# Optimization experiments

Hardware: AMD Instinct MI355X
Metric: run time of the kernel (lower is better)

The kernel has to match this reference:

```python
import jax, jax.numpy as jnp
import numpy as np

EPS = 1e-5
L = 256
CHANNELS = 256


def setup_inputs() -> dict:
    key = jax.random.key(0)
    ks = jax.random.split(key, 7)
    B, C, D, H, W = 2, 256, 48, 48, 48
    x = jax.random.normal(ks[0], (B, C, D, H, W), dtype=jnp.float32)
    # Conv1d(kernel=1) weights: [out_channels, in_channels], plus bias.
    s = 1.0 / np.sqrt(C)
    Wq = jax.random.uniform(ks[1], (CHANNELS, C), jnp.float32, -s, s)
    bq = jax.random.uniform(ks[2], (CHANNELS,), jnp.float32, -s, s)
    Wk = jax.random.uniform(ks[3], (CHANNELS, C), jnp.float32, -s, s)
    bk = jax.random.uniform(ks[4], (CHANNELS,), jnp.float32, -s, s)
    Wv = jax.random.uniform(ks[5], (CHANNELS, C), jnp.float32, -s, s)
    bv = jax.random.uniform(ks[6], (CHANNELS,), jnp.float32, -s, s)
    outer = jnp.eye(L, dtype=jnp.float32)  # learned, init = identity
    return {"x": x, "Wq": Wq, "bq": bq, "Wk": Wk, "bk": bk, "Wv": Wv, "bv": bv, "outer": outer}


def reference(x, Wq, bq, Wk, bk, Wv, bv, outer):
    B, C, D, H, W = x.shape
    N = D * H * W
    # InstanceNorm3d (affine=False): normalize per (B, C) over spatial dims, biased var.
    xf = x.reshape(B, C, N)
    mean = jnp.mean(xf, axis=-1, keepdims=True)
    var = jnp.mean(jnp.square(xf - mean), axis=-1, keepdims=True)
    xn = (xf - mean) * jax.lax.rsqrt(var + EPS)  # [B, C, N]
    # 1x1 Conv1d projections == GEMM over channel dim.
    q = jnp.einsum('oc,bcn->bon', Wq, xn) + bq[None, :, None]
    k = jnp.einsum('oc,bcn->bon', Wk, xn) + bk[None, :, None]
    v = jnp.einsum('oc,bcn->bon', Wv, xn) + bv[None, :, None]
    # Channel attention: scores [B, C, C]; scale applied AFTER softmax.
    scores = jnp.einsum('bcn,bdn->bcd', q, k)
    atten = jax.nn.softmax(scores, axis=-1) / jnp.sqrt(jnp.float32(CHANNELS))
    atten = atten + (outer / jnp.sqrt(jnp.float32(L)))[None, :, :]
    out = jnp.einsum('bcd,bdn->bcn', atten, v)
    # Residual is to the NORMALIZED x (x was reassigned in the original forward).
    return (out + xn).reshape(B, C, D, H, W)
```

## Files before the change

### kernel.cpp

```cpp
#include <hip/hip_runtime.h>
#include <hip/hip_bf16.h>

#define B_ 2
#define C_ 256
#define N_ 110592
#define CN_ ((size_t)C_ * N_)
#define NCK_ 128
#define TW_ 32
#define T_ 27

typedef __attribute__((ext_vector_type(4))) float f32x4;
typedef __attribute__((ext_vector_type(8))) short bf16x8;
typedef __attribute__((ext_vector_type(4))) short bf16x4;

__device__ __forceinline__ short f2bf(float f) {
    union { float f; unsigned u; } v; v.f = f;
    unsigned r = (v.u + 0x7fffu + ((v.u >> 16) & 1u)) >> 16;
    return (short)(r & 0xffffu);
}

__device__ __forceinline__ void gload16f(const float* g, float* l) {
    __builtin_amdgcn_global_load_lds(
        (const __attribute__((address_space(1))) void*)g,
        (__attribute__((address_space(3))) void*)l, 16, 0, 0);
}

__device__ __forceinline__ void gload16s(const short* g, short* l) {
    __builtin_amdgcn_global_load_lds(
        (const __attribute__((address_space(1))) void*)g,
        (__attribute__((address_space(3))) void*)l, 16, 0, 0);
}

__global__ __launch_bounds__(1024, 4) void k_gram(
        const float* __restrict__ x, float* __restrict__ part,
        float* __restrict__ rspart, short* __restrict__ xf, int wxf) {
    __shared__ float Xf[3 * 8192];
    __shared__ short Xb[256 * 40];
    __shared__ float rs_s[256];
    const int t = threadIdx.x, lane = t & 63, wave = t >> 6;
    const int chunk = blockIdx.x, b = blockIdx.y;
    const int k0 = chunk * (T_ * TW_);
    const int cw0 = (wave & 3) * 64, dw0 = (wave >> 2) * 64;
    const int r16 = lane & 15, g16 = lane >> 4;
    const float* xb = x + (size_t)b * CN_;
    short* xfb = xf + (size_t)b * CN_;

    const int s_row = t >> 3;
    const int g_src = (t & 7) ^ (s_row & 7);
    const int rp_r = t >> 2, rp_q = t & 3;
    const int rp_g0 = (2 * rp_q) ^ (rp_r & 7);
    const int em_cg = t >> 5, em_nn = t & 31;

    f32x4 acc[4][4];
#pragma unroll
    for (int i = 0; i < 4; ++i)
#pragma unroll
        for (int j = 0; j < 4; ++j) acc[i][j] = f32x4{0.f, 0.f, 0.f, 0.f};
    float rs = 0.f;

#define GSTAGE(TT, BB)                                                        \
    {                                                                         \
        const float* gsrc = xb + k0 + (TT) * TW_ + g_src * 4;                 \
        float* ldst = Xf + (BB) * 8192;                                       \
        gload16f(gsrc + (size_t)s_row * N_, ldst + t * 4);                    \
        gload16f(gsrc + (size_t)(s_row + 128) * N_, ldst + (t + 1024) * 4);   \
    }

    GSTAGE(0, 0)
    GSTAGE(1, 1)

    int bb = 0;
    for (int tt = 0; tt < T_; ++tt) {
        asm volatile("s_waitcnt vmcnt(2)" ::: "memory");
        __builtin_amdgcn_s_barrier();
        if (tt + 2 < T_) {
            int bn = bb + 2; if (bn >= 3) bn -= 3;
            GSTAGE(tt + 2, bn)
        }
        {
            const float* src = Xf + bb * 8192 + rp_r * 32;
            f32x4 a = *(const f32x4*)(src + rp_g0 * 4);
            f32x4 c = *(const f32x4*)(src + (rp_g0 ^ 1) * 4);
            rs += ((a.x + a.y) + (a.z + a.w)) + ((c.x + c.y) + (c.z + c.w));
            bf16x8 h;
            h[0] = f2bf(a.x); h[1] = f2bf(a.y); h[2] = f2bf(a.z); h[3] = f2bf(a.w);
            h[4] = f2bf(c.x); h[5] = f2bf(c.y); h[6] = f2bf(c.z); h[7] = f2bf(c.w);
            *(bf16x8*)(Xb + rp_r * 40 + rp_q * 8) = h;
        }
        asm volatile("s_waitcnt lgkmcnt(0)" ::: "memory");
        __builtin_amdgcn_s_barrier();
        {
            bf16x8 afr[4];
#pragma unroll
            for (int ct = 0; ct < 4; ++ct)
                afr[ct] = *(const bf16x8*)(Xb + (cw0 + ct * 16 + r16) * 40 + g16 * 8);
#pragma unroll
            for (int dt = 0; dt < 4; ++dt) {
                bf16x8 bfr = *(const bf16x8*)(Xb + (dw0 + dt * 16 + r16) * 40 + g16 * 8);
#pragma unroll
                for (int ct = 0; ct < 4; ++ct)
                    acc[ct][dt] = __builtin_amdgcn_mfma_f32_16x16x32_bf16(
                        afr[ct], bfr, acc[ct][dt], 0, 0, 0);
            }
        }
        if (wxf) {
            bf16x8 h;
#pragma unroll
            for (int j = 0; j < 8; ++j)
                h[j] = Xb[(em_cg * 8 + j) * 40 + em_nn];
            *(bf16x8*)(xfb + ((size_t)em_cg * N_ + k0 + tt * TW_ + em_nn) * 8) = h;
        }
        ++bb; if (bb >= 3) bb -= 3;
    }
#undef GSTAGE

    rs += __shfl_xor(rs, 1);
    rs += __shfl_xor(rs, 2);
    if (rp_q == 0) rs_s[rp_r] = rs;
    __syncthreads();
    if (t < 256) rspart[((size_t)b * NCK_ + chunk) * C_ + t] = rs_s[t];

    float* pp = part + ((size_t)b * NCK_ + chunk) * (C_ * C_);
#pragma unroll
    for (int ct = 0; ct < 4; ++ct)
#pragma unroll
        for (int dt = 0; dt < 4; ++dt) {
            int d = dw0 + dt * 16 + r16;
#pragma unroll
            for (int rr = 0; rr < 4; ++rr) {
                int c = cw0 + ct * 16 + g16 * 4 + rr;
                pp[(size_t)c * C_ + d] = acc[ct][dt][rr];
            }
        }
}

__global__ void k_reduce(const float* __restrict__ part, const float* __restrict__ rspart,
                         float* __restrict__ Graw, float* __restrict__ mean,
                         float* __restrict__ rsig) {
    __shared__ float diag_s;
    __shared__ float red[256];
    int bid = blockIdx.x;
    int b = bid >> 8, c = bid & 255;
    int d = threadIdx.x;
    float s = 0.f;
    for (int p = 0; p < NCK_; ++p)
        s += part[(((size_t)b * NCK_ + p) * (C_ * C_)) + (size_t)c * C_ + d];
    Graw[((size_t)b * C_ + c) * C_ + d] = s;
    if (d == c) diag_s = s;
    float rsum = 0.f;
    for (int p = d; p < NCK_; p += 256)
        rsum += rspart[((size_t)b * NCK_ + p) * C_ + c];
    red[d] = rsum;
    __syncthreads();
    if (d < 128) red[d] += red[d + 128];
    __syncthreads();
    if (d < 64) red[d] += red[d + 64];
    __syncthreads();
    if (d == 0) {
        float tot = 0.f;
#pragma unroll
        for (int i = 0; i < 64; ++i) tot += red[i];
        float m = tot / (float)N_;
        float var = diag_s / (float)N_ - m * m;
        mean[b * C_ + c] = m;
        rsig[b * C_ + c] = rsqrtf(var + 1e-5f);
    }
}

__global__ void k_gemm1(const float* __restrict__ Wq, const float* __restrict__ Graw,
                        const float* __restrict__ mean, const float* __restrict__ rsig,
                        float* __restrict__ P) {
    int bid = blockIdx.x; int b = bid >> 8, c = bid & 255; int d = threadIdx.x;
    const float* G = Graw + (size_t)b * C_ * C_;
    const float* mb = mean + b * C_;
    const float* rb = rsig + b * C_;
    float md = mb[d], rd = rb[d];
    float a1 = 0.f, a2 = 0.f;
    for (int e = 0; e < C_; ++e) {
        float w = Wq[(size_t)c * C_ + e] * rb[e];
        a1 += w * G[(size_t)e * C_ + d];
        a2 += w * mb[e];
    }
    P[((size_t)b * C_ + c) * C_ + d] = rd * a1 - (float)N_ * md * rd * a2;
}

__global__ void k_attn(const float* __restrict__ P, const float* __restrict__ Wk,
                       const float* __restrict__ bq, const float* __restrict__ bk,
                       const float* __restrict__ outer, float* __restrict__ atten) {
    __shared__ float Pr_s[256];
    __shared__ float red[8];
    int bid = blockIdx.x; int b = bid >> 8, c = bid & 255; int d = threadIdx.x;
    int lane = d & 63, w = d >> 6;
    Pr_s[d] = P[((size_t)b * C_ + c) * C_ + d];
    __syncthreads();
    float a = 0.f;
#pragma unroll 4
    for (int e4 = 0; e4 < 64; ++e4) {
        f32x4 wv = *(const f32x4*)(Wk + (size_t)d * C_ + e4 * 4);
        f32x4 pv = *(const f32x4*)(Pr_s + e4 * 4);
        a += wv.x * pv.x + wv.y * pv.y + wv.z * pv.z + wv.w * pv.w;
    }
    float v = a + (float)N_ * bq[c] * bk[d];
    float m = v;
    for (int off = 32; off; off >>= 1) m = fmaxf(m, __shfl_xor(m, off));
    if (lane == 0) red[w] = m;
    __syncthreads();
    m = fmaxf(fmaxf(red[0], red[1]), fmaxf(red[2], red[3]));
    float e = __expf(v - m);
    float s = e;
    for (int off = 32; off; off >>= 1) s += __shfl_xor(s, off);
    if (lane == 0) red[4 + w] = s;
    __syncthreads();
    s = red[4] + red[5] + red[6] + red[7];
    atten[((size_t)b * C_ + c) * C_ + d] = e / (s * 16.f) + outer[(size_t)c * C_ + d] * 0.0625f;
}

__global__ void k_gemm3(const float* __restrict__ atten, const float* __restrict__ Wv,
                        const float* __restrict__ bv, const float* __restrict__ mean,
                        const float* __restrict__ rsig, short* __restrict__ Abf,
                        float* __restrict__ beta) {
    __shared__ float red[4];
    int bid = blockIdx.x; int b = bid >> 8, c = bid & 255; int g = threadIdx.x;
    int lane = g & 63, w = g >> 6;
    const float* at = atten + ((size_t)b * C_ + c) * C_;
    float a = 0.f;
    for (int d = 0; d < C_; ++d)
        a += at[d] * Wv[(size_t)d * C_ + g];
    float Ag = (a + ((g == c) ? 1.f : 0.f)) * rsig[b * C_ + g];
    Abf[(size_t)b * C_ * C_ + ((size_t)(g >> 3) * C_ + c) * 8 + (g & 7)] = f2bf(Ag);
    float u = at[g] * bv[g] - Ag * mean[b * C_ + g];
    for (int off = 32; off; off >>= 1) u += __shfl_xor(u, off);
    if (lane == 0) red[w] = u;
    __syncthreads();
    if (g == 0) beta[b * C_ + c] = red[0] + red[1] + red[2] + red[3];
}

__global__ __launch_bounds__(512, 4) void k_out2(
        const short* __restrict__ xf, const short* __restrict__ Abf,
        const float* __restrict__ beta, float* __restrict__ out) {
    __shared__ short Xt[2 * 8192];
    __shared__ float Wb[8 * 32 * 33];
    const int t = threadIdx.x, lane = t & 63, wave = t >> 6;
    const int nb = blockIdx.x, b = blockIdx.y;
    const int col = lane & 15, g16 = lane >> 4;
    const int cw0 = wave * 32;
    const int r8 = lane >> 3, s8 = lane & 7;
    const int n_blk = nb * 256;
    const short* Ab = Abf + (size_t)b * C_ * C_;
    const short* xfb = xf + (size_t)b * CN_;
    float* ob = out + (size_t)b * CN_;
    float* wl = Wb + wave * (32 * 33);

    bf16x8 Af[2][8];
#pragma unroll
    for (int ct = 0; ct < 2; ++ct)
#pragma unroll
        for (int ks = 0; ks < 8; ++ks)
            Af[ct][ks] = *(const bf16x8*)(Ab +
                ((size_t)((ks * 4 + g16) * 256 + cw0 + ct * 16 + col)) * 8);
    float bet[4];
#pragma unroll
    for (int j = 0; j < 4; ++j) bet[j] = beta[b * C_ + cw0 + j * 8 + r8];

#define STAGE(BUF, N0)                                                        \
    {                                                                         \
        _Pragma("unroll")                                                     \
        for (int r = 0; r < 2; ++r) {                                         \
            int s = r * 512 + t;                                              \
            int kg = s >> 5, nsl = s & 31;                                    \
            int nn = nsl ^ (kg & 3);                                          \
            gload16s(xfb + ((size_t)kg * N_ + (N0) + nn) * 8,                 \
                     Xt + (BUF) * 8192 + s * 8);                              \
        }                                                                     \
    }

    STAGE(0, n_blk)
    __syncthreads();

    for (int it = 0; it < 8; ++it) {
        const int cur = it & 1;
        if (it + 1 < 8) STAGE(cur ^ 1, n_blk + (it + 1) * 32)
        const int n0 = n_blk + it * 32;

        f32x4 acc[2][2];
#pragma unroll
        for (int i = 0; i < 2; ++i) {
            acc[i][0] = f32x4{0.f, 0.f, 0.f, 0.f};
            acc[i][1] = f32x4{0.f, 0.f, 0.f, 0.f};
        }
#pragma unroll
        for (int ks = 0; ks < 8; ++ks) {
            const int kg = ks * 4 + g16;
            bf16x8 x0 = *(const bf16x8*)(Xt + cur * 8192 +
                                         (kg * 32 + (col ^ (kg & 3))) * 8);
            bf16x8 x1 = *(const bf16x8*)(Xt + cur * 8192 +
                                         (kg * 32 + ((16 + col) ^ (kg & 3))) * 8);
            acc[0][0] = __builtin_amdgcn_mfma_f32_16x16x32_bf16(Af[0][ks], x0, acc[0][0], 0, 0, 0);
            acc[1][0] = __builtin_amdgcn_mfma_f32_16x16x32_bf16(Af[1][ks], x0, acc[1][0], 0, 0, 0);
            acc[0][1] = __builtin_amdgcn_mfma_f32_16x16x32_bf16(Af[0][ks], x1, acc[0][1], 0, 0, 0);
            acc[1][1] = __builtin_amdgcn_mfma_f32_16x16x32_bf16(Af[1][ks], x1, acc[1][1], 0, 0, 0);
        }
#pragma unroll
        for (int ct = 0; ct < 2; ++ct)
#pragma unroll
            for (int nt = 0; nt < 2; ++nt)
#pragma unroll
                for (int rr = 0; rr < 4; ++rr)
                    wl[(ct * 16 + g16 * 4 + rr) * 33 + nt * 16 + col] = acc[ct][nt][rr];
#pragma unroll
        for (int j = 0; j < 4; ++j) {
            f32x4 v = *(const f32x4*)(wl + (j * 8 + r8) * 33 + s8 * 4);
            float bb = bet[j];
            v.x += bb; v.y += bb; v.z += bb; v.w += bb;
            *(f32x4*)(ob + (size_t)(cw0 + j * 8 + r8) * N_ + n0 + s8 * 4) = v;
        }
        __syncthreads();
    }
#undef STAGE
}

__global__ __launch_bounds__(512) void k_out_f32(
        const float* __restrict__ x, const short* __restrict__ Abf,
        const float* __restrict__ beta, float* __restrict__ out) {
    __shared__ float beta_s[256];
    const int t = threadIdx.x, lane = t & 63, wave = t >> 6;
    const int nb = blockIdx.x, b = blockIdx.y;
    const int col = lane & 15, g16 = lane >> 4;
    const int n_w = nb * 256 + wave * 32;
    if (t < 256) beta_s[t] = beta[b * C_ + t];
    __syncthreads();
    const short* Ab = Abf + (size_t)b * C_ * C_;
    const float* xb = x + (size_t)b * CN_;
    float* ob = out + (size_t)b * CN_;

    f32x4 acc[16][2];
#pragma unroll
    for (int i = 0; i < 16; ++i) {
        acc[i][0] = f32x4{0.f, 0.f, 0.f, 0.f};
        acc[i][1] = f32x4{0.f, 0.f, 0.f, 0.f};
    }
    float pf[2][16];
#define XL(KS, NT, J) xb[(size_t)((KS)*32 + g16 * 8 + (J)) * N_ + n_w + (NT)*16 + col]
#pragma unroll
    for (int j = 0; j < 8; ++j) { pf[0][j] = XL(0, 0, j); pf[0][8 + j] = XL(0, 1, j); }
#pragma unroll
    for (int ks = 0; ks < 8; ++ks) {
        if (ks + 1 < 8) {
#pragma unroll
            for (int j = 0; j < 8; ++j) {
                pf[(ks + 1) & 1][j] = XL(ks + 1, 0, j);
                pf[(ks + 1) & 1][8 + j] = XL(ks + 1, 1, j);
            }
        }
        bf16x8 xa, xv;
#pragma unroll
        for (int j = 0; j < 8; ++j) {
            xa[j] = f2bf(pf[ks & 1][j]);
            xv[j] = f2bf(pf[ks & 1][8 + j]);
        }
#pragma unroll
        for (int ct = 0; ct < 16; ++ct) {
            bf16x8 afr = *(const bf16x8*)(Ab + ((size_t)((ks * 4 + g16) * 256 + ct * 16 + col)) * 8);
            acc[ct][0] = __builtin_amdgcn_mfma_f32_16x16x32_bf16(afr, xa, acc[ct][0], 0, 0, 0);
            acc[ct][1] = __builtin_amdgcn_mfma_f32_16x16x32_bf16(afr, xv, acc[ct][1], 0, 0, 0);
        }
    }
#undef XL
#pragma unroll
    for (int ct = 0; ct < 16; ++ct)
#pragma unroll
        for (int nt = 0; nt < 2; ++nt) {
            int n = n_w + nt * 16 + col;
#pragma unroll
            for (int rr = 0; rr < 4; ++rr) {
                int c = ct * 16 + g16 * 4 + rr;
                ob[(size_t)c * N_ + n] = acc[ct][nt][rr] + beta_s[c];
            }
        }
}

extern "C" void kernel_launch(void* const* d_in, const int* in_sizes, int n_in,
                              void* d_out, int out_size, void* d_ws, size_t ws_size,
                              hipStream_t stream) {
    (void)in_sizes; (void)n_in; (void)out_size;
    const float* x     = (const float*)d_in[0];
    const float* Wq    = (const float*)d_in[1];
    const float* bq    = (const float*)d_in[2];
    const float* Wk    = (const float*)d_in[3];
    const float* bk    = (const float*)d_in[4];
    const float* Wv    = (const float*)d_in[5];
    const float* bv    = (const float*)d_in[6];
    const float* outer = (const float*)d_in[7];
    float* out = (float*)d_out;

    char* w = (char*)d_ws;
    float* mean   = (float*)(w + 0);
    float* rsig   = (float*)(w + 2048);
    float* beta   = (float*)(w + 4096);
    float* rspart = (float*)(w + 8192);
    float* Graw   = (float*)(w + 270336);
    float* P      = (float*)(w + 794624);
    float* atten  = (float*)(w + 1318912);
    short* Abf    = (short*)(w + 1843200);
    const size_t fixed = 2105344;
    const size_t part_bytes = (size_t)NCK_ * B_ * C_ * C_ * 4;
    const size_t xf_bytes = (size_t)B_ * CN_ * 2;
    float* part = (float*)(w + fixed);
    short* xf   = (short*)(w + fixed + part_bytes);

    const bool big = ws_size >= fixed + part_bytes + xf_bytes;

    k_gram  <<<dim3(NCK_, B_), 1024, 0, stream>>>(x, part, rspart, xf, big ? 1 : 0);
    k_reduce<<<dim3(B_ * C_), 256, 0, stream>>>(part, rspart, Graw, mean, rsig);
    k_gemm1 <<<dim3(B_ * C_), C_, 0, stream>>>(Wq, Graw, mean, rsig, P);
    k_attn  <<<dim3(B_ * C_), C_, 0, stream>>>(P, Wk, bq, bk, outer, atten);
    k_gemm3 <<<dim3(B_ * C_), C_, 0, stream>>>(atten, Wv, bv, mean, rsig, Abf, beta);
    if (big) {
        k_out2  <<<dim3(N_ / 256, B_), 512, 0, stream>>>(xf, Abf, beta, out);
    } else {
        k_out_f32<<<dim3(N_ / 256, B_), 512, 0, stream>>>(x, Abf, beta, out);
    }
}
```

Before: 229.0 us.

## Split Gram stage into bf16 prep pass, bf16-fed Gram GEMM, vectorized reduce

Adds a k_prep kernel that reads fp32 x once, computes per-row sums, and writes two bf16 copies: a tile-contiguous layout for the Gram GEMM and the existing layout for the output stage. The Gram kernel then streams pre-tiled bf16 tiles with a single async load per thread, with no in-loop fp32-to-bf16 conversion or strided global access. The reduction is vectorized with float4 loads split across four thread groups. The cost is an extra 113 MB bf16 write plus an extra launch, traded for cheaper, better-pipelined Gram loads.

```diff
diff --git a/kernel.cpp b/kernel.cpp
--- a/kernel.cpp
+++ b/kernel.cpp
@@ -6,7 +6,6 @@
 #define N_ 110592
 #define CN_ ((size_t)C_ * N_)
 #define NCK_ 128
-#define TW_ 32
 #define T_ 27
 
 typedef __attribute__((ext_vector_type(4))) float f32x4;
@@ -31,25 +30,184 @@
         (__attribute__((address_space(3))) void*)l, 16, 0, 0);
 }
 
-__global__ __launch_bounds__(1024, 4) void k_gram(
+__global__ __launch_bounds__(256) void k_prep(
+        const float* __restrict__ x, short* __restrict__ xg,
+        short* __restrict__ xf, float* __restrict__ rs2) {
+    __shared__ float Xs[64 * 256];
+    __shared__ float rsum_s[64];
+    const int t = threadIdx.x;
+    const int nb = blockIdx.x, q = blockIdx.y, b = blockIdx.z;
+    const int c0 = q * 64, n0 = nb * 1536;
+    const float* xb = x + (size_t)b * CN_;
+    short* xgb = xg + (size_t)b * CN_;
+    short* xfb = xf + (size_t)b * CN_;
+    const int rr = t >> 2, qq = t & 3;
+    const int kgl = t >> 5, nl = t & 31;
+    float racc = 0.f;
+
+    for (int sl = 0; sl < 6; ++sl) {
+#pragma unroll
+        for (int r = 0; r < 16; ++r) {
+            int slot = r * 256 + t;
+            int row = slot >> 6, c4 = slot & 63;
+            gload16f(xb + (size_t)(c0 + row) * N_ + n0 + sl * 256 + c4 * 4,
+                     Xs + slot * 4);
+        }
+        __syncthreads();
+        {
+            const f32x4* src = (const f32x4*)(Xs + rr * 256 + qq * 64);
+#pragma unroll
+            for (int j = 0; j < 16; ++j) {
+                f32x4 v = src[j];
+                racc += (v.x + v.y) + (v.z + v.w);
+            }
+        }
+#pragma unroll
+        for (int tau = 0; tau < 8; ++tau) {
+            int gl = qq ^ (rr & 3);
+            const float* s2 = Xs + rr * 256 + tau * 32 + gl * 8;
+            bf16x8 h;
+#pragma unroll
+            for (int e = 0; e < 8; ++e) h[e] = f2bf(s2[e]);
+            size_t tg = (size_t)(nb * 48 + sl * 8 + tau);
+            *(bf16x8*)(xgb + tg * 8192 + (c0 + rr) * 32 + qq * 8) = h;
+        }
+#pragma unroll
+        for (int nn = 0; nn < 8; ++nn) {
+            bf16x8 h;
+#pragma unroll
+            for (int j = 0; j < 8; ++j)
+                h[j] = f2bf(Xs[(kgl * 8 + j) * 256 + nn * 32 + nl]);
+            *(bf16x8*)(xfb + ((size_t)(q * 8 + kgl) * N_ +
+                              n0 + sl * 256 + nn * 32 + nl) * 8) = h;
+        }
+        __syncthreads();
+    }
+    racc += __shfl_xor(racc, 1);
+    racc += __shfl_xor(racc, 2);
+    if ((t & 3) == 0) rsum_s[t >> 2] = racc;
+    __syncthreads();
+    if (t < 64)
+        rs2[((size_t)b * C_ + c0 + t) * 72 + nb] = rsum_s[t];
+}
+
+__global__ __launch_bounds__(1024, 4) void k_gram_bf(
+        const short* __restrict__ xg, float* __restrict__ part) {
+    __shared__ short Xs[3 * 8192];
+    const int t = threadIdx.x, lane = t & 63, wave = t >> 6;
+    const int chunk = blockIdx.x, b = blockIdx.y;
+    const int cw0 = (wave & 3) * 64, dw0 = (wave >> 2) * 64;
+    const int r16 = lane & 15, g16 = lane >> 4;
+    const int gsw = g16 ^ (r16 & 3);
+    const short* xgb = xg + (size_t)b * CN_ + (size_t)chunk * T_ * 8192;
+
+    f32x4 acc[4][4];
+#pragma unroll
+    for (int i = 0; i < 4; ++i)
+#pragma unroll
+        for (int j = 0; j < 4; ++j) acc[i][j] = f32x4{0.f, 0.f, 0.f, 0.f};
+
+#define GST(TT, BB) gload16s(xgb + (size_t)(TT) * 8192 + t * 8, Xs + (BB) * 8192 + t * 8);
+
+    GST(0, 0)
+    GST(1, 1)
+
+    int bb = 0;
+    for (int tt = 0; tt < T_; ++tt) {
+        if (tt + 1 < T_) asm volatile("s_waitcnt vmcnt(1)" ::: "memory");
+        else             asm volatile("s_waitcnt vmcnt(0)" ::: "memory");
+        __builtin_amdgcn_sched_barrier(0);
+        __builtin_amdgcn_s_barrier();
+        if (tt + 2 < T_) {
+            int bn = bb + 2; if (bn >= 3) bn -= 3;
+            GST(tt + 2, bn)
+        }
+        const short* base = Xs + bb * 8192;
+        bf16x8 afr[4];
+#pragma unroll
+        for (int ct = 0; ct < 4; ++ct)
+            afr[ct] = *(const bf16x8*)(base + (cw0 + ct * 16 + r16) * 32 + gsw * 8);
+#pragma unroll
+        for (int dt = 0; dt < 4; ++dt) {
+            bf16x8 bfr = *(const bf16x8*)(base + (dw0 + dt * 16 + r16) * 32 + gsw * 8);
+#pragma unroll
+            for (int ct = 0; ct < 4; ++ct)
+                acc[ct][dt] = __builtin_amdgcn_mfma_f32_16x16x32_bf16(
+                    afr[ct], bfr, acc[ct][dt], 0, 0, 0);
+        }
+        asm volatile("s_waitcnt lgkmcnt(0)" ::: "memory");
+        __builtin_amdgcn_sched_barrier(0);
+        ++bb; if (bb >= 3) bb -= 3;
+    }
+#undef GST
+
+    float* pp = part + ((size_t)b * NCK_ + chunk) * (C_ * C_);
+#pragma unroll
+    for (int ct = 0; ct < 4; ++ct)
+#pragma unroll
+        for (int dt = 0; dt < 4; ++dt) {
+            int d = dw0 + dt * 16 + r16;
+#pragma unroll
+            for (int rr = 0; rr < 4; ++rr) {
+                int c = cw0 + ct * 16 + g16 * 4 + rr;
+                pp[(size_t)c * C_ + d] = acc[ct][dt][rr];
+            }
+        }
+}
+
+__global__ void k_reduce2(const float* __restrict__ part, const float* __restrict__ rs2,
+                          float* __restrict__ Graw, float* __restrict__ mean,
+                          float* __restrict__ rsig) {
+    __shared__ f32x4 red[4 * 64];
+    __shared__ float rsr[72];
+    __shared__ float diag_s;
+    int bid = blockIdx.x;
+    int b = bid >> 8, c = bid & 255;
+    int t = threadIdx.x;
+    int dq = t & 63, ps = t >> 6;
+    f32x4 s = f32x4{0.f, 0.f, 0.f, 0.f};
+    for (int p = ps; p < NCK_; p += 4)
+        s += *(const f32x4*)(part + (((size_t)b * NCK_ + p) * (C_ * C_)) +
+                             (size_t)c * C_ + dq * 4);
+    red[ps * 64 + dq] = s;
+    if (t < 72) rsr[t] = rs2[((size_t)b * C_ + c) * 72 + t];
+    __syncthreads();
+    if (t < 64) {
+        f32x4 a = red[t] + red[64 + t] + red[128 + t] + red[192 + t];
+        *(f32x4*)(Graw + ((size_t)b * C_ + c) * C_ + t * 4) = a;
+        if (t == (c >> 2)) {
+            int m3 = c & 3;
+            diag_s = (m3 == 0) ? a.x : ((m3 == 1) ? a.y : ((m3 == 2) ? a.z : a.w));
+        }
+    }
+    __syncthreads();
+    if (t == 0) {
+        float tot = 0.f;
+#pragma unroll
+        for (int i = 0; i < 72; ++i) tot += rsr[i];
+        float m = tot / (float)N_;
+        float var = diag_s / (float)N_ - m * m;
+        mean[b * C_ + c] = m;
+        rsig[b * C_ + c] = rsqrtf(var + 1e-5f);
+    }
+}
+
+__global__ __launch_bounds__(1024, 4) void k_gram_fb(
         const float* __restrict__ x, float* __restrict__ part,
-        float* __restrict__ rspart, short* __restrict__ xf, int wxf) {
+        float* __restrict__ rspart) {
     __shared__ float Xf[3 * 8192];
     __shared__ short Xb[256 * 40];
     __shared__ float rs_s[256];
     const int t = threadIdx.x, lane = t & 63, wave = t >> 6;
     const int chunk = blockIdx.x, b = blockIdx.y;
-    const int k0 = chunk * (T_ * TW_);
+    const int k0 = chunk * (T_ * 32);
     const int cw0 = (wave & 3) * 64, dw0 = (wave >> 2) * 64;
     const int r16 = lane & 15, g16 = lane >> 4;
     const float* xb = x + (size_t)b * CN_;
-    short* xfb = xf + (size_t)b * CN_;
-
     const int s_row = t >> 3;
     const int g_src = (t & 7) ^ (s_row & 7);
     const int rp_r = t >> 2, rp_q = t & 3;
     const int rp_g0 = (2 * rp_q) ^ (rp_r & 7);
-    const int em_cg = t >> 5, em_nn = t & 31;
 
     f32x4 acc[4][4];
 #pragma unroll
@@ -60,18 +218,17 @@
 
 #define GSTAGE(TT, BB)                                                        \
     {                                                                         \
-        const float* gsrc = xb + k0 + (TT) * TW_ + g_src * 4;                 \
+        const float* gsrc = xb + k0 + (TT) * 32 + g_src * 4;                  \
         float* ldst = Xf + (BB) * 8192;                                       \
         gload16f(gsrc + (size_t)s_row * N_, ldst + t * 4);                    \
         gload16f(gsrc + (size_t)(s_row + 128) * N_, ldst + (t + 1024) * 4);   \
     }
-
     GSTAGE(0, 0)
     GSTAGE(1, 1)
-
     int bb = 0;
     for (int tt = 0; tt < T_; ++tt) {
-        asm volatile("s_waitcnt vmcnt(2)" ::: "memory");
+        if (tt + 1 < T_) asm volatile("s_waitcnt vmcnt(2)" ::: "memory");
+        else             asm volatile("s_waitcnt vmcnt(0)" ::: "memory");
         __builtin_amdgcn_s_barrier();
         if (tt + 2 < T_) {
             int bn = bb + 2; if (bn >= 3) bn -= 3;
@@ -103,23 +260,14 @@
                         afr[ct], bfr, acc[ct][dt], 0, 0, 0);
             }
         }
-        if (wxf) {
-            bf16x8 h;
-#pragma unroll
-            for (int j = 0; j < 8; ++j)
-                h[j] = Xb[(em_cg * 8 + j) * 40 + em_nn];
-            *(bf16x8*)(xfb + ((size_t)em_cg * N_ + k0 + tt * TW_ + em_nn) * 8) = h;
-        }
         ++bb; if (bb >= 3) bb -= 3;
     }
 #undef GSTAGE
-
     rs += __shfl_xor(rs, 1);
     rs += __shfl_xor(rs, 2);
     if (rp_q == 0) rs_s[rp_r] = rs;
     __syncthreads();
     if (t < 256) rspart[((size_t)b * NCK_ + chunk) * C_ + t] = rs_s[t];
-
     float* pp = part + ((size_t)b * NCK_ + chunk) * (C_ * C_);
 #pragma unroll
     for (int ct = 0; ct < 4; ++ct)
@@ -134,9 +282,9 @@
         }
 }
 
-__global__ void k_reduce(const float* __restrict__ part, const float* __restrict__ rspart,
-                         float* __restrict__ Graw, float* __restrict__ mean,
-                         float* __restrict__ rsig) {
+__global__ void k_reduce_fb(const float* __restrict__ part, const float* __restrict__ rspart,
+                            float* __restrict__ Graw, float* __restrict__ mean,
+                            float* __restrict__ rsig) {
     __shared__ float diag_s;
     __shared__ float red[256];
     int bid = blockIdx.x;
@@ -397,6 +545,7 @@
     float* mean   = (float*)(w + 0);
     float* rsig   = (float*)(w + 2048);
     float* beta   = (float*)(w + 4096);
+    float* rs2    = (float*)(w + 8192);
     float* rspart = (float*)(w + 8192);
     float* Graw   = (float*)(w + 270336);
     float* P      = (float*)(w + 794624);
@@ -405,13 +554,21 @@
     const size_t fixed = 2105344;
     const size_t part_bytes = (size_t)NCK_ * B_ * C_ * C_ * 4;
     const size_t xf_bytes = (size_t)B_ * CN_ * 2;
+    const size_t xg_bytes = (size_t)B_ * CN_ * 2;
     float* part = (float*)(w + fixed);
     short* xf   = (short*)(w + fixed + part_bytes);
-
-    const bool big = ws_size >= fixed + part_bytes + xf_bytes;
-
-    k_gram  <<<dim3(NCK_, B_), 1024, 0, stream>>>(x, part, rspart, xf, big ? 1 : 0);
-    k_reduce<<<dim3(B_ * C_), 256, 0, stream>>>(part, rspart, Graw, mean, rsig);
+    short* xg   = (short*)(w + fixed + part_bytes + xf_bytes);
+
+    const bool big = ws_size >= fixed + part_bytes + xf_bytes + xg_bytes;
+
+    if (big) {
+        k_prep   <<<dim3(72, 4, B_), 256, 0, stream>>>(x, xg, xf, rs2);
+        k_gram_bf<<<dim3(NCK_, B_), 1024, 0, stream>>>(xg, part);
+        k_reduce2<<<dim3(B_ * C_), 256, 0, stream>>>(part, rs2, Graw, mean, rsig);
+    } else {
+        k_gram_fb  <<<dim3(NCK_, B_), 1024, 0, stream>>>(x, part, rspart);
+        k_reduce_fb<<<dim3(B_ * C_), 256, 0, stream>>>(part, rspart, Graw, mean, rsig);
+    }
     k_gemm1 <<<dim3(B_ * C_), C_, 0, stream>>>(Wq, Graw, mean, rsig, P);
     k_attn  <<<dim3(B_ * C_), C_, 0, stream>>>(P, Wk, bq, bk, outer, atten);
     k_gemm3 <<<dim3(B_ * C_), C_, 0, stream>>>(atten, Wv, bv, mean, rsig, Abf, beta);
```

Result: slower. 288.2 us (+25.9%).
